# Kernel tuning notes

Measured on AMD Instinct MI355X. Metric: run time of the kernel, lower is better.

Reference implementation:

```python
import jax, jax.numpy as jnp
import numpy as np

N = 50000   # nodes
HID = 32    # hidden_channels
H = 8       # heads == num_edge_features (positional-arg aliasing in source)
E = 800000  # message-passing edges
L = 100000  # supervision (label) edges
NEG_SLOPE = 0.2


def gat_layer(x, src, dst, edge_attr, W, a_src, a_dst, We, a_e, b):
    # x: [N, Fin]; W: [Fin, H*C] -> out [N, H*C] (concat heads), PyG GATConv math
    C = W.shape[1] // H
    h = (x @ W).reshape(-1, H, C)                 # [N, H, C]
    al_src = (h * a_src).sum(-1)                  # [N, H]
    al_dst = (h * a_dst).sum(-1)                  # [N, H]
    he = (edge_attr @ We).reshape(-1, H, C)       # [E, H, C]
    al_e = (he * a_e).sum(-1)                     # [E, H]
    alpha = al_src[src] + al_dst[dst] + al_e      # [E, H]
    alpha = jax.nn.leaky_relu(alpha, NEG_SLOPE)
    # segment softmax over destination-node neighborhoods
    amax = jax.ops.segment_max(alpha, dst, num_segments=N)
    amax = jnp.where(jnp.isfinite(amax), amax, 0.0)
    ex = jnp.exp(alpha - amax[dst])
    denom = jax.ops.segment_sum(ex, dst, num_segments=N)
    w = ex / (denom[dst] + 1e-16)                 # [E, H]
    out = jax.ops.segment_sum(h[src] * w[:, :, None], dst, num_segments=N)
    return out.reshape(-1, H * C) + b             # [N, H*C]


def setup_inputs():
    key = jax.random.key(0)
    ks = jax.random.split(key, 24)
    s = 0.1
    d = {}
    d["node_ids"] = jax.random.randint(ks[0], (N,), 0, N)
    d["edge_index"] = jax.random.randint(ks[1], (2, E), 0, N)
    d["edge_label_index"] = jax.random.randint(ks[2], (2, L), 0, N)
    d["topic"] = jax.random.randint(ks[3], (1,), 0, 10)
    d["edge_attr"] = jax.random.normal(ks[4], (E, H))
    d["edge_label_attr"] = jax.random.normal(ks[5], (L, H))
    d["emb"] = jax.random.normal(ks[6], (N, HID)) * s
    d["W1"] = jax.random.normal(ks[7], (HID, H * HID)) * s
    d["a_src1"] = jax.random.normal(ks[8], (H, HID)) * s
    d["a_dst1"] = jax.random.normal(ks[9], (H, HID)) * s
    d["We1"] = jax.random.normal(ks[10], (H, H * HID)) * s
    d["a_e1"] = jax.random.normal(ks[11], (H, HID)) * s
    d["b1"] = jnp.zeros((H * HID,))
    d["lin1_W"] = jax.random.normal(ks[12], (H * HID, HID)) * s
    d["lin1_b"] = jnp.zeros((HID,))
    d["W2"] = jax.random.normal(ks[13], (HID, H * HID)) * s
    d["a_src2"] = jax.random.normal(ks[14], (H, HID)) * s
    d["a_dst2"] = jax.random.normal(ks[15], (H, HID)) * s
    d["We2"] = jax.random.normal(ks[16], (H, H * HID)) * s
    d["a_e2"] = jax.random.normal(ks[17], (H, HID)) * s
    d["b2"] = jnp.zeros((H * HID,))
    d["lin5_W"] = jax.random.normal(ks[18], (H * HID, H)) * s
    d["lin5_b"] = jnp.zeros((H,))
    d["clf_W"] = jax.random.normal(ks[19], (2 * H, H)) * s
    d["clf_b"] = jnp.zeros((H,))
    return d


def reference(node_ids, edge_index, edge_label_index, topic, edge_attr, edge_label_attr, emb, W1, a_src1, a_dst1, We1, a_e1, b1, lin1_W, lin1_b, W2, a_src2, a_dst2, We2, a_e2, b2, lin5_W, lin5_b, clf_W, clf_b):
    src, dst = edge_index[0], edge_index[1]
    x = emb[node_ids]                                                   # [N, HID]
    x = jax.nn.relu(gat_layer(x, src, dst, edge_attr, W1, a_src1, a_dst1, We1, a_e1, b1))
    x = x @ lin1_W + lin1_b                                             # dropout(p=0.1) is identity in eval
    x = jax.nn.relu(gat_layer(x, src, dst, edge_attr, W2, a_src2, a_dst2, We2, a_e2, b2))
    x = x @ lin5_W + lin5_b                                             # [N, H]
    fu = x[edge_label_index[0]]                                         # [L, H]
    fm = x[edge_label_index[1]]                                         # [L, H]
    fu = jnp.concatenate([fu, edge_label_attr], axis=-1) @ clf_W + clf_b
    return jax.nn.sigmoid((fu * fm).sum(-1))                            # [L]
```

## Files before the change

### kernel.cpp

```cpp
#include <hip/hip_runtime.h>
#include <hip/hip_bf16.h>

#define HC    256
#define FIN   32
#define NH    8
#define GROUP 8
#define CAPW  32

typedef __hip_bfloat16 bf16;

__device__ __forceinline__ float blo(unsigned int u) { return __uint_as_float(u << 16); }
__device__ __forceinline__ float bhi(unsigned int u) { return __uint_as_float(u & 0xffff0000u); }

__global__ void count_kernel(const int* __restrict__ dst, int* __restrict__ cnt, int E_) {
  int e = blockIdx.x * blockDim.x + threadIdx.x;
  if (e < E_) atomicAdd(&cnt[dst[e]], 1);
}

__global__ __launch_bounds__(256) void
scan_partial(const int* __restrict__ cnt, int* __restrict__ tmp,
             int* __restrict__ bsum, int N_) {
  __shared__ int part[256];
  int t = threadIdx.x, i = blockIdx.x * 256 + t;
  int v = (i < N_) ? cnt[i] : 0;
  part[t] = v;
  __syncthreads();
#pragma unroll
  for (int off = 1; off < 256; off <<= 1) {
    int u = (t >= off) ? part[t - off] : 0;
    __syncthreads();
    part[t] += u;
    __syncthreads();
  }
  if (i < N_) tmp[i] = part[t];
  if (t == 255) bsum[blockIdx.x] = part[255];
}

__global__ __launch_bounds__(1024) void
scan_bsum(int* __restrict__ bsum, int NB) {
  __shared__ int part[1024];
  int t = threadIdx.x;
  int v = (t < NB) ? bsum[t] : 0;
  part[t] = v;
  __syncthreads();
  for (int off = 1; off < 1024; off <<= 1) {
    int u = (t >= off) ? part[t - off] : 0;
    __syncthreads();
    part[t] += u;
    __syncthreads();
  }
  if (t < NB) bsum[t] = part[t] - v;
}

__global__ __launch_bounds__(256) void
scan_final(const int* __restrict__ cnt, const int* __restrict__ tmp,
           const int* __restrict__ bsum, int* __restrict__ rowptr,
           int* __restrict__ fill, int N_, int E_) {
  int t = threadIdx.x, i = blockIdx.x * 256 + t;
  if (i < N_) {
    int ex = bsum[blockIdx.x] + tmp[i] - cnt[i];
    rowptr[i] = ex;
    fill[i] = ex;
  }
  if (i == 0) rowptr[N_] = E_;
}

__global__ void scatter_kernel(const int* __restrict__ src, const int* __restrict__ dst,
                               int* __restrict__ fill, const float* __restrict__ edge_attr,
                               const float* __restrict__ M,
                               int* __restrict__ srcs, float* __restrict__ ale1,
                               float* __restrict__ ale2, int E_) {
  __shared__ float Msh[128];
  if (threadIdx.x < 128) Msh[threadIdx.x] = M[threadIdx.x];
  __syncthreads();
  int e = blockIdx.x * blockDim.x + threadIdx.x;
  if (e < E_) {
    int pos = atomicAdd(&fill[dst[e]], 1);
    srcs[pos] = src[e];
    const float4* ep = (const float4*)(edge_attr + (size_t)e * NH);
    float4 a0 = ep[0], a1 = ep[1];
    float ea[8] = {a0.x, a0.y, a0.z, a0.w, a1.x, a1.y, a1.z, a1.w};
    float o1[8], o2[8];
#pragma unroll
    for (int h = 0; h < 8; ++h) { o1[h] = 0.f; o2[h] = 0.f; }
#pragma unroll
    for (int k = 0; k < 8; ++k) {
      float x = ea[k];
#pragma unroll
      for (int h = 0; h < 8; ++h) {
        o1[h] = fmaf(x, Msh[k * 8 + h], o1[h]);
        o2[h] = fmaf(x, Msh[64 + k * 8 + h], o2[h]);
      }
    }
    float4* p1 = (float4*)(ale1 + (size_t)pos * NH);
    p1[0] = make_float4(o1[0], o1[1], o1[2], o1[3]);
    p1[1] = make_float4(o1[4], o1[5], o1[6], o1[7]);
    float4* p2 = (float4*)(ale2 + (size_t)pos * NH);
    p2[0] = make_float4(o2[0], o2[1], o2[2], o2[3]);
    p2[1] = make_float4(o2[4], o2[5], o2[6], o2[7]);
  }
}

__global__ void fold_kernel(const float* __restrict__ We1, const float* __restrict__ ae1,
                            const float* __restrict__ We2, const float* __restrict__ ae2,
                            const float* __restrict__ W1, const float* __restrict__ as1,
                            const float* __restrict__ ad1,
                            const float* __restrict__ W2, const float* __restrict__ as2,
                            const float* __restrict__ ad2,
                            float* __restrict__ M) {
  for (int idx = threadIdx.x; idx < 1152; idx += 256) {
    const float* A; const float* V; int i;
    if (idx < 64)       { i = idx;       A = We1; V = ae1; }
    else if (idx < 128) { i = idx - 64;  A = We2; V = ae2; }
    else if (idx < 384) { i = idx - 128; A = W1;  V = as1; }
    else if (idx < 640) { i = idx - 384; A = W1;  V = ad1; }
    else if (idx < 896) { i = idx - 640; A = W2;  V = as2; }
    else                { i = idx - 896; A = W2;  V = ad2; }
    int k = i >> 3, h = i & 7;
    float s = 0.f;
    for (int c = 0; c < FIN; ++c)
      s = fmaf(A[k * HC + h * FIN + c], V[h * FIN + c], s);
    M[idx] = s;
  }
}

__global__ __launch_bounds__(256) void
prep1_kernel(const float* __restrict__ emb, const int* __restrict__ node_ids,
             const float* __restrict__ P,
             bf16* __restrict__ xq, float* __restrict__ alsrc,
             float* __restrict__ aldst, int N_) {
  __shared__ float xs[8][33];
  int t = threadIdx.x, n0 = blockIdx.x * 8;
  int nl = t >> 5, c = t & 31;
  int n = n0 + nl;
  if (n < N_) {
    float v = emb[(size_t)node_ids[n] * FIN + c];
    xq[(size_t)n * FIN + c] = __float2bfloat16(v);
    xs[nl][c] = v;
  }
  __syncthreads();
  if (t < 64) {
    int nl2 = t >> 3, h = t & 7;
    int n2 = n0 + nl2;
    if (n2 < N_) {
      float sa = 0.f, sd = 0.f;
#pragma unroll
      for (int k = 0; k < FIN; ++k) {
        float x = xs[nl2][k];
        sa = fmaf(x, P[k * 8 + h], sa);
        sd = fmaf(x, P[256 + k * 8 + h], sd);
      }
      alsrc[(size_t)n2 * NH + h] = sa;
      aldst[(size_t)n2 * NH + h] = sd;
    }
  }
}

template <int K, int LOG2K, bool LOGITS>
__global__ __launch_bounds__(256, 8) void
agg_kernel(const int* __restrict__ rowptr, const int* __restrict__ srcs,
           const float* __restrict__ ale,
           const float* __restrict__ alsrc, const float* __restrict__ aldst,
           const bf16* __restrict__ xq,
           const float* __restrict__ W, const float* __restrict__ b,
           const float* __restrict__ Wlin, const float* __restrict__ blin,
           float* __restrict__ xoutf, bf16* __restrict__ xqn,
           const float* __restrict__ Pn,
           float* __restrict__ alsrcn, float* __restrict__ aldstn, int N_) {
  __shared__ __align__(16) char smem[17408];
  unsigned int* xsu = (unsigned int*)smem;
  float* wsf   = (float*)(smem + 8192);
  float* ald_s = (float*)(smem + 12288);
  float* zs   = (float*)smem;
  float* gs   = (float*)(smem + 8192);
  float* red  = (float*)smem;
  float* xrow = (float*)(smem + 16384);

  int t = threadIdx.x;
  int n0 = blockIdx.x * GROUP;
  int w = t >> 6, l = t & 63, h = l >> 3, q = l & 7;

  unsigned int* xw  = xsu + w * 512;
  float*        wsw = wsf + w * 256;

  int nA = n0 + w * 2;
  int e0  = rowptr[(nA     <= N_) ? nA     : N_];
  int e1  = rowptr[(nA + 1 <= N_) ? nA + 1 : N_];
  int e2g = rowptr[(nA + 2 <= N_) ? nA + 2 : N_];

  if (t < GROUP * NH) {
    int nn = n0 + (t >> 3);
    ald_s[t] = (nn < N_) ? aldst[(size_t)nn * NH + (t & 7)] : 0.f;
  }
  __syncthreads();

  float4 acc0 = make_float4(0.f, 0.f, 0.f, 0.f);
  float4 acc1 = make_float4(0.f, 0.f, 0.f, 0.f);
  float dn0 = 0.f, dn1 = 0.f;

  for (int cbeg = e0; cbeg < e2g; cbeg += CAPW) {
    int clen = e2g - cbeg; if (clen > CAPW) clen = CAPW;

    int ntask = clen * 8;
    for (int idx = l; idx < ntask; idx += 64) {
      int e = idx >> 3, c4 = idx & 7;
      int s = srcs[cbeg + e];
      uint2 v = *(const uint2*)(xq + (size_t)s * FIN + c4 * 4);
      *(uint2*)&xw[e * 16 + c4 * 2] = v;
    }
    {
      int e2 = l >> 1, half = l & 1;
      if (e2 < clen) {
        int j = cbeg + e2;
        int ii = (j >= e1) ? 1 : 0;
        int sn = srcs[j];
        float4 av  = *(const float4*)(ale + (size_t)j * NH + half * 4);
        float4 as4 = *(const float4*)(alsrc + (size_t)sn * NH + half * 4);
        float4 ad4 = *(const float4*)&ald_s[(w * 2 + ii) * 8 + half * 4];
        float o[4];
        float a0f = av.x + as4.x + ad4.x; a0f = (a0f >= 0.f) ? a0f : 0.2f * a0f;
        float a1f = av.y + as4.y + ad4.y; a1f = (a1f >= 0.f) ? a1f : 0.2f * a1f;
        float a2f = av.z + as4.z + ad4.z; a2f = (a2f >= 0.f) ? a2f : 0.2f * a2f;
        float a3f = av.w + as4.w + ad4.w; a3f = (a3f >= 0.f) ? a3f : 0.2f * a3f;
        o[0] = __expf(a0f); o[1] = __expf(a1f); o[2] = __expf(a2f); o[3] = __expf(a3f);
        *(float4*)&wsw[e2 * 8 + half * 4] = make_float4(o[0], o[1], o[2], o[3]);
      }
    }
    asm volatile("s_waitcnt lgkmcnt(0)" ::: "memory");

    int hA = e1 - cbeg; if (hA < 0) hA = 0; if (hA > clen) hA = clen;
#pragma unroll 4
    for (int le = 0; le < hA; ++le) {
      float wv = wsw[le * 8 + h];
      uint2 u = *(const uint2*)&xw[le * 16 + q * 2];
      acc0.x = fmaf(blo(u.x), wv, acc0.x);
      acc0.y = fmaf(bhi(u.x), wv, acc0.y);
      acc0.z = fmaf(blo(u.y), wv, acc0.z);
      acc0.w = fmaf(bhi(u.y), wv, acc0.w);
      dn0 += wv;
    }
#pragma unroll 4
    for (int le = hA; le < clen; ++le) {
      float wv = wsw[le * 8 + h];
      uint2 u = *(const uint2*)&xw[le * 16 + q * 2];
      acc1.x = fmaf(blo(u.x), wv, acc1.x);
      acc1.y = fmaf(bhi(u.x), wv, acc1.y);
      acc1.z = fmaf(blo(u.y), wv, acc1.z);
      acc1.w = fmaf(bhi(u.y), wv, acc1.w);
      dn1 += wv;
    }
    asm volatile("s_waitcnt lgkmcnt(0)" ::: "memory");
  }

  float rd0 = 1.0f / (dn0 + 1e-16f);
  float rd1 = 1.0f / (dn1 + 1e-16f);
  *(float4*)&zs[(w * 2 + 0) * 256 + l * 4] =
      make_float4(acc0.x * rd0, acc0.y * rd0, acc0.z * rd0, acc0.w * rd0);
  *(float4*)&zs[(w * 2 + 1) * 256 + l * 4] =
      make_float4(acc1.x * rd1, acc1.y * rd1, acc1.z * rd1, acc1.w * rd1);
  __syncthreads();

  int hE = t >> 5;
  float g[GROUP];
#pragma unroll
  for (int i = 0; i < GROUP; ++i) g[i] = b[t];
#pragma unroll
  for (int k4 = 0; k4 < 8; ++k4) {
    float za[GROUP][4];
#pragma unroll
    for (int i = 0; i < GROUP; ++i)
      *(float4*)za[i] = *(const float4*)&zs[i * 256 + hE * 32 + k4 * 4];
#pragma unroll
    for (int kk = 0; kk < 4; ++kk) {
      float wv = W[(k4 * 4 + kk) * HC + t];
#pragma unroll
      for (int i = 0; i < GROUP; ++i) g[i] = fmaf(za[i][kk], wv, g[i]);
    }
  }
  __syncthreads();
#pragma unroll
  for (int i = 0; i < GROUP; ++i) gs[i * 256 + t] = (g[i] > 0.f) ? g[i] : 0.f;
  __syncthreads();

  {
    int kk = t & (K - 1), r = t >> LOG2K;
    float part[GROUP];
#pragma unroll
    for (int i = 0; i < GROUP; ++i) part[i] = 0.f;
#pragma unroll
    for (int j4 = 0; j4 < K / 4; ++j4) {
      float ga[GROUP][4];
#pragma unroll
      for (int i = 0; i < GROUP; ++i)
        *(float4*)ga[i] = *(const float4*)&gs[i * 256 + r * K + j4 * 4];
#pragma unroll
      for (int jj = 0; jj < 4; ++jj) {
        float wl = Wlin[(r * K + j4 * 4 + jj) * K + kk];
#pragma unroll
        for (int i = 0; i < GROUP; ++i) part[i] = fmaf(ga[i][jj], wl, part[i]);
      }
    }
#pragma unroll
    for (int i = 0; i < GROUP; ++i) red[i * 256 + t] = part[i];
  }
  __syncthreads();

  if (LOGITS) {
    if (t < GROUP * 32) {
      int i = t >> 5, kk = t & 31;
      float s = blin[kk];
#pragma unroll
      for (int r2 = 0; r2 < HC / K; ++r2) s += red[i * 256 + r2 * K + kk];
      int nn = n0 + i;
      if (nn < N_) xqn[(size_t)nn * FIN + kk] = __float2bfloat16(s);
      xrow[t] = s;
    }
    __syncthreads();
    if (t < GROUP * NH) {
      int i = t >> 3, hh = t & 7;
      int nn = n0 + i;
      if (nn < N_) {
        float sa = 0.f, sd = 0.f;
#pragma unroll
        for (int k2 = 0; k2 < FIN; ++k2) {
          float x = xrow[i * 32 + k2];
          sa = fmaf(x, Pn[k2 * 8 + hh], sa);
          sd = fmaf(x, Pn[256 + k2 * 8 + hh], sd);
        }
        alsrcn[(size_t)nn * NH + hh] = sa;
        aldstn[(size_t)nn * NH + hh] = sd;
      }
    }
  } else {
    if (t < GROUP * K) {
      int i = t >> LOG2K, kk = t & (K - 1);
      float s = blin[kk];
#pragma unroll
      for (int r2 = 0; r2 < HC / K; ++r2) s += red[i * 256 + r2 * K + kk];
      int nn = n0 + i;
      if (nn < N_) xoutf[(size_t)nn * K + kk] = s;
    }
  }
}

__global__ void clf_kernel(const int* __restrict__ eli, const float* __restrict__ ela,
                           const float* __restrict__ x2, const float* __restrict__ clfW,
                           const float* __restrict__ clfb, float* __restrict__ out, int L_) {
  int i = blockIdx.x * blockDim.x + threadIdx.x;
  if (i >= L_) return;
  int u = eli[i], m = eli[L_ + i];
  const float4* xup = (const float4*)(x2 + (size_t)u * NH);
  const float4* xmp = (const float4*)(x2 + (size_t)m * NH);
  const float4* eap = (const float4*)(ela + (size_t)i * NH);
  float4 xu0 = xup[0], xu1 = xup[1];
  float4 xm0 = xmp[0], xm1 = xmp[1];
  float4 el0 = eap[0], el1 = eap[1];
  float xu[NH] = {xu0.x, xu0.y, xu0.z, xu0.w, xu1.x, xu1.y, xu1.z, xu1.w};
  float xm[NH] = {xm0.x, xm0.y, xm0.z, xm0.w, xm1.x, xm1.y, xm1.z, xm1.w};
  float el[NH] = {el0.x, el0.y, el0.z, el0.w, el1.x, el1.y, el1.z, el1.w};
  float fu[NH];
#pragma unroll
  for (int kk = 0; kk < NH; ++kk) fu[kk] = clfb[kk];
#pragma unroll
  for (int j = 0; j < NH; ++j) {
#pragma unroll
    for (int kk = 0; kk < NH; ++kk) fu[kk] = fmaf(xu[j], clfW[j * NH + kk], fu[kk]);
  }
#pragma unroll
  for (int j = 0; j < NH; ++j) {
#pragma unroll
    for (int kk = 0; kk < NH; ++kk) fu[kk] = fmaf(el[j], clfW[(NH + j) * NH + kk], fu[kk]);
  }
  float dot = 0.f;
#pragma unroll
  for (int kk = 0; kk < NH; ++kk) dot += fu[kk] * xm[kk];
  out[i] = 1.f / (1.f + expf(-dot));
}

extern "C" void kernel_launch(void* const* d_in, const int* in_sizes, int n_in,
                              void* d_out, int out_size, void* d_ws, size_t ws_size,
                              hipStream_t stream) {
  const int* node_ids   = (const int*)d_in[0];
  const int* edge_index = (const int*)d_in[1];
  const int* eli        = (const int*)d_in[2];
  const float* edge_attr = (const float*)d_in[4];
  const float* ela       = (const float*)d_in[5];
  const float* emb       = (const float*)d_in[6];
  const float* W1     = (const float*)d_in[7];
  const float* a_src1 = (const float*)d_in[8];
  const float* a_dst1 = (const float*)d_in[9];
  const float* We1    = (const float*)d_in[10];
  const float* a_e1   = (const float*)d_in[11];
  const float* b1     = (const float*)d_in[12];
  const float* lin1W  = (const float*)d_in[13];
  const float* lin1b  = (const float*)d_in[14];
  const float* W2     = (const float*)d_in[15];
  const float* a_src2 = (const float*)d_in[16];
  const float* a_dst2 = (const float*)d_in[17];
  const float* We2    = (const float*)d_in[18];
  const float* a_e2   = (const float*)d_in[19];
  const float* b2     = (const float*)d_in[20];
  const float* lin5W  = (const float*)d_in[21];
  const float* lin5b  = (const float*)d_in[22];
  const float* clfW   = (const float*)d_in[23];
  const float* clfb   = (const float*)d_in[24];

  const int N_ = in_sizes[0];
  const int E_ = in_sizes[1] / 2;
  const int L_ = in_sizes[2] / 2;
  const int* src  = edge_index;
  const int* dstp = edge_index + E_;

  char* p = (char*)d_ws;
  auto carve = [&](size_t bytes) -> char* {
    char* r = p;
    p += (bytes + 255) & ~(size_t)255;
    return r;
  };
  bf16*  xq1     = (bf16*)carve((size_t)N_ * FIN * 2);
  bf16*  xq2     = (bf16*)carve((size_t)N_ * FIN * 2);
  float* ale1_s  = (float*)carve((size_t)E_ * NH * 4);
  float* ale2_s  = (float*)carve((size_t)E_ * NH * 4);
  float* alsrc1  = (float*)carve((size_t)N_ * NH * 4);
  float* aldst1  = (float*)carve((size_t)N_ * NH * 4);
  float* alsrc2  = (float*)carve((size_t)N_ * NH * 4);
  float* aldst2  = (float*)carve((size_t)N_ * NH * 4);
  float* x2b     = (float*)carve((size_t)N_ * NH * 4);
  float* Mbuf    = (float*)carve(1152 * 4);
  int*   cnt     = (int*)carve((size_t)N_ * 4);
  int*   rowptr  = (int*)carve((size_t)(N_ + 1) * 4);
  int*   fill    = (int*)carve((size_t)N_ * 4);
  int*   stmp    = (int*)carve((size_t)N_ * 4);
  int*   bsum    = (int*)carve(1024 * 4);
  int*   srcs    = (int*)carve((size_t)E_ * 4);

  hipMemsetAsync(cnt, 0, (size_t)N_ * 4, stream);
  int eb = (E_ + 255) / 256;
  int nb = (N_ + 255) / 256;
  fold_kernel<<<1, 256, 0, stream>>>(We1, a_e1, We2, a_e2, W1, a_src1, a_dst1,
                                     W2, a_src2, a_dst2, Mbuf);
  count_kernel<<<eb, 256, 0, stream>>>(dstp, cnt, E_);
  scan_partial<<<nb, 256, 0, stream>>>(cnt, stmp, bsum, N_);
  scan_bsum<<<1, 1024, 0, stream>>>(bsum, nb);
  scan_final<<<nb, 256, 0, stream>>>(cnt, stmp, bsum, rowptr, fill, N_, E_);
  scatter_kernel<<<eb, 256, 0, stream>>>(src, dstp, fill, edge_attr, Mbuf,
                                         srcs, ale1_s, ale2_s, E_);
  prep1_kernel<<<(N_ + 7) / 8, 256, 0, stream>>>(emb, node_ids, Mbuf + 128,
                                                 xq1, alsrc1, aldst1, N_);

  int gb = (N_ + GROUP - 1) / GROUP;
  agg_kernel<32, 5, true><<<gb, 256, 0, stream>>>(
      rowptr, srcs, ale1_s, alsrc1, aldst1, xq1,
      W1, b1, lin1W, lin1b, nullptr, xq2, Mbuf + 640, alsrc2, aldst2, N_);

  agg_kernel<8, 3, false><<<gb, 256, 0, stream>>>(
      rowptr, srcs, ale2_s, alsrc2, aldst2, xq2,
      W2, b2, lin5W, lin5b, x2b, nullptr, nullptr, nullptr, nullptr, N_);

  clf_kernel<<<(L_ + 255) / 256, 256, 0, stream>>>(eli, ela, x2b, clfW, clfb,
                                                   (float*)d_out, L_);
}
```

Measured before the change: 365.5 us.

## Fuse preprocessing kernels, drop fill atomics, store edge logits as bf16

count_kernel now saves each edge's atomic slot order, so the scatter step can compute its CSR position as rowptr plus that order without a second atomic pass. The fold computation moves into the single-block bsum scan kernel, and the edge scatter and node prep are merged into one launch split by block index. Edge attention logits for both layers are packed as bf16 into one interleaved 32-byte record, halving that storage and its read traffic in the aggregation kernels. The trade-offs are an extra ord array write and read, and reduced precision on the edge logit term.

After: 330.2 us. -9.6%, faster.

```diff
diff --git a/kernel.cpp b/kernel.cpp
--- a/kernel.cpp
+++ b/kernel.cpp
@@ -11,10 +11,17 @@
 
 __device__ __forceinline__ float blo(unsigned int u) { return __uint_as_float(u << 16); }
 __device__ __forceinline__ float bhi(unsigned int u) { return __uint_as_float(u & 0xffff0000u); }
-
-__global__ void count_kernel(const int* __restrict__ dst, int* __restrict__ cnt, int E_) {
+__device__ __forceinline__ unsigned int pk2(float a, float b) {
+  bf16 ha = __float2bfloat16(a), hb = __float2bfloat16(b);
+  unsigned short ua, ub;
+  __builtin_memcpy(&ua, &ha, 2); __builtin_memcpy(&ub, &hb, 2);
+  return (unsigned int)ua | ((unsigned int)ub << 16);
+}
+
+__global__ void count_kernel(const int* __restrict__ dst, int* __restrict__ cnt,
+                             int* __restrict__ ord, int E_) {
   int e = blockIdx.x * blockDim.x + threadIdx.x;
-  if (e < E_) atomicAdd(&cnt[dst[e]], 1);
+  if (e < E_) ord[e] = atomicAdd(&cnt[dst[e]], 1);
 }
 
 __global__ __launch_bounds__(256) void
@@ -37,7 +44,14 @@
 }
 
 __global__ __launch_bounds__(1024) void
-scan_bsum(int* __restrict__ bsum, int NB) {
+scan_bsum_fold(int* __restrict__ bsum, int NB,
+               const float* __restrict__ We1, const float* __restrict__ ae1,
+               const float* __restrict__ We2, const float* __restrict__ ae2,
+               const float* __restrict__ W1, const float* __restrict__ as1,
+               const float* __restrict__ ad1,
+               const float* __restrict__ W2, const float* __restrict__ as2,
+               const float* __restrict__ ad2,
+               float* __restrict__ M) {
   __shared__ int part[1024];
   int t = threadIdx.x;
   int v = (t < NB) ? bsum[t] : 0;
@@ -50,65 +64,8 @@
     __syncthreads();
   }
   if (t < NB) bsum[t] = part[t] - v;
-}
-
-__global__ __launch_bounds__(256) void
-scan_final(const int* __restrict__ cnt, const int* __restrict__ tmp,
-           const int* __restrict__ bsum, int* __restrict__ rowptr,
-           int* __restrict__ fill, int N_, int E_) {
-  int t = threadIdx.x, i = blockIdx.x * 256 + t;
-  if (i < N_) {
-    int ex = bsum[blockIdx.x] + tmp[i] - cnt[i];
-    rowptr[i] = ex;
-    fill[i] = ex;
-  }
-  if (i == 0) rowptr[N_] = E_;
-}
-
-__global__ void scatter_kernel(const int* __restrict__ src, const int* __restrict__ dst,
-                               int* __restrict__ fill, const float* __restrict__ edge_attr,
-                               const float* __restrict__ M,
-                               int* __restrict__ srcs, float* __restrict__ ale1,
-                               float* __restrict__ ale2, int E_) {
-  __shared__ float Msh[128];
-  if (threadIdx.x < 128) Msh[threadIdx.x] = M[threadIdx.x];
-  __syncthreads();
-  int e = blockIdx.x * blockDim.x + threadIdx.x;
-  if (e < E_) {
-    int pos = atomicAdd(&fill[dst[e]], 1);
-    srcs[pos] = src[e];
-    const float4* ep = (const float4*)(edge_attr + (size_t)e * NH);
-    float4 a0 = ep[0], a1 = ep[1];
-    float ea[8] = {a0.x, a0.y, a0.z, a0.w, a1.x, a1.y, a1.z, a1.w};
-    float o1[8], o2[8];
-#pragma unroll
-    for (int h = 0; h < 8; ++h) { o1[h] = 0.f; o2[h] = 0.f; }
-#pragma unroll
-    for (int k = 0; k < 8; ++k) {
-      float x = ea[k];
-#pragma unroll
-      for (int h = 0; h < 8; ++h) {
-        o1[h] = fmaf(x, Msh[k * 8 + h], o1[h]);
-        o2[h] = fmaf(x, Msh[64 + k * 8 + h], o2[h]);
-      }
-    }
-    float4* p1 = (float4*)(ale1 + (size_t)pos * NH);
-    p1[0] = make_float4(o1[0], o1[1], o1[2], o1[3]);
-    p1[1] = make_float4(o1[4], o1[5], o1[6], o1[7]);
-    float4* p2 = (float4*)(ale2 + (size_t)pos * NH);
-    p2[0] = make_float4(o2[0], o2[1], o2[2], o2[3]);
-    p2[1] = make_float4(o2[4], o2[5], o2[6], o2[7]);
-  }
-}
-
-__global__ void fold_kernel(const float* __restrict__ We1, const float* __restrict__ ae1,
-                            const float* __restrict__ We2, const float* __restrict__ ae2,
-                            const float* __restrict__ W1, const float* __restrict__ as1,
-                            const float* __restrict__ ad1,
-                            const float* __restrict__ W2, const float* __restrict__ as2,
-                            const float* __restrict__ ad2,
-                            float* __restrict__ M) {
-  for (int idx = threadIdx.x; idx < 1152; idx += 256) {
+
+  for (int idx = t; idx < 1152; idx += 1024) {
     const float* A; const float* V; int i;
     if (idx < 64)       { i = idx;       A = We1; V = ae1; }
     else if (idx < 128) { i = idx - 64;  A = We2; V = ae2; }
@@ -125,33 +82,80 @@
 }
 
 __global__ __launch_bounds__(256) void
-prep1_kernel(const float* __restrict__ emb, const int* __restrict__ node_ids,
-             const float* __restrict__ P,
-             bf16* __restrict__ xq, float* __restrict__ alsrc,
-             float* __restrict__ aldst, int N_) {
+scan_final(const int* __restrict__ cnt, const int* __restrict__ tmp,
+           const int* __restrict__ bsum, int* __restrict__ rowptr,
+           int N_, int E_) {
+  int t = threadIdx.x, i = blockIdx.x * 256 + t;
+  if (i < N_) rowptr[i] = bsum[blockIdx.x] + tmp[i] - cnt[i];
+  if (i == 0) rowptr[N_] = E_;
+}
+
+__global__ __launch_bounds__(256) void
+scatter_prep_kernel(const int* __restrict__ src, const int* __restrict__ dst,
+                    const int* __restrict__ rowptr, const int* __restrict__ ord,
+                    const float* __restrict__ edge_attr, const float* __restrict__ M,
+                    int* __restrict__ srcs, unsigned int* __restrict__ alepk,
+                    const float* __restrict__ emb, const int* __restrict__ node_ids,
+                    bf16* __restrict__ xq, float* __restrict__ alsrc,
+                    float* __restrict__ aldst,
+                    int E_, int N_, int eb) {
+  __shared__ float Msh[128];
   __shared__ float xs[8][33];
-  int t = threadIdx.x, n0 = blockIdx.x * 8;
-  int nl = t >> 5, c = t & 31;
-  int n = n0 + nl;
-  if (n < N_) {
-    float v = emb[(size_t)node_ids[n] * FIN + c];
-    xq[(size_t)n * FIN + c] = __float2bfloat16(v);
-    xs[nl][c] = v;
-  }
-  __syncthreads();
-  if (t < 64) {
-    int nl2 = t >> 3, h = t & 7;
-    int n2 = n0 + nl2;
-    if (n2 < N_) {
-      float sa = 0.f, sd = 0.f;
-#pragma unroll
-      for (int k = 0; k < FIN; ++k) {
-        float x = xs[nl2][k];
-        sa = fmaf(x, P[k * 8 + h], sa);
-        sd = fmaf(x, P[256 + k * 8 + h], sd);
+  int t = threadIdx.x;
+  if (blockIdx.x < eb) {
+    if (t < 128) Msh[t] = M[t];
+    __syncthreads();
+    int e = blockIdx.x * 256 + t;
+    if (e < E_) {
+      int pos = rowptr[dst[e]] + ord[e];
+      srcs[pos] = src[e];
+      const float4* ep = (const float4*)(edge_attr + (size_t)e * NH);
+      float4 a0 = ep[0], a1 = ep[1];
+      float ea[8] = {a0.x, a0.y, a0.z, a0.w, a1.x, a1.y, a1.z, a1.w};
+      float o1[8], o2[8];
+#pragma unroll
+      for (int h = 0; h < 8; ++h) { o1[h] = 0.f; o2[h] = 0.f; }
+#pragma unroll
+      for (int k = 0; k < 8; ++k) {
+        float x = ea[k];
+#pragma unroll
+        for (int h = 0; h < 8; ++h) {
+          o1[h] = fmaf(x, Msh[k * 8 + h], o1[h]);
+          o2[h] = fmaf(x, Msh[64 + k * 8 + h], o2[h]);
+        }
       }
-      alsrc[(size_t)n2 * NH + h] = sa;
-      aldst[(size_t)n2 * NH + h] = sd;
+      uint4 r0 = make_uint4(pk2(o1[0], o1[1]), pk2(o1[2], o1[3]),
+                            pk2(o1[4], o1[5]), pk2(o1[6], o1[7]));
+      uint4 r1 = make_uint4(pk2(o2[0], o2[1]), pk2(o2[2], o2[3]),
+                            pk2(o2[4], o2[5]), pk2(o2[6], o2[7]));
+      uint4* op = (uint4*)(alepk + (size_t)pos * 8);
+      op[0] = r0; op[1] = r1;
+    }
+  } else {
+    const float* P = M + 128;
+    int n0 = (blockIdx.x - eb) * 8;
+    int nl = t >> 5, c = t & 31;
+    int n = n0 + nl;
+    if (n < N_) {
+      float v = emb[(size_t)node_ids[n] * FIN + c];
+      xq[(size_t)n * FIN + c] = __float2bfloat16(v);
+      xs[nl][c] = v;
+    }
+    __syncthreads();
+    if (t < 64) {
+      int nl2 = t >> 3, h = t & 7;
+      int n2 = n0 + nl2;
+      if (n2 < N_) {
+        float sa = 0.f, sd = 0.f;
+#pragma unroll
+        for (int k = 0; k < FIN; ++k) {
+          float x = xs[nl2][k];
+          sa = fmaf(x, P[k * 8 + h], sa);
+          sd = fmaf(x, P[256 + k * 8 + h], sd);
+        }
+        alsrc[(size_t)n2 * NH + h] = sa;
+        aldst[(size_t)n2 * NH + h] = sd;
+      }
     }
   }
 }
@@ -159,7 +163,7 @@
 template <int K, int LOG2K, bool LOGITS>
 __global__ __launch_bounds__(256, 8) void
 agg_kernel(const int* __restrict__ rowptr, const int* __restrict__ srcs,
-           const float* __restrict__ ale,
+           const bf16* __restrict__ ale,
            const float* __restrict__ alsrc, const float* __restrict__ aldst,
            const bf16* __restrict__ xq,
            const float* __restrict__ W, const float* __restrict__ b,
@@ -214,16 +218,15 @@
         int j = cbeg + e2;
         int ii = (j >= e1) ? 1 : 0;
         int sn = srcs[j];
-        float4 av  = *(const float4*)(ale + (size_t)j * NH + half * 4);
+        uint2 ue  = *(const uint2*)(ale + (size_t)j * 16 + half * 4);
         float4 as4 = *(const float4*)(alsrc + (size_t)sn * NH + half * 4);
         float4 ad4 = *(const float4*)&ald_s[(w * 2 + ii) * 8 + half * 4];
-        float o[4];
-        float a0f = av.x + as4.x + ad4.x; a0f = (a0f >= 0.f) ? a0f : 0.2f * a0f;
-        float a1f = av.y + as4.y + ad4.y; a1f = (a1f >= 0.f) ? a1f : 0.2f * a1f;
-        float a2f = av.z + as4.z + ad4.z; a2f = (a2f >= 0.f) ? a2f : 0.2f * a2f;
-        float a3f = av.w + as4.w + ad4.w; a3f = (a3f >= 0.f) ? a3f : 0.2f * a3f;
-        o[0] = __expf(a0f); o[1] = __expf(a1f); o[2] = __expf(a2f); o[3] = __expf(a3f);
-        *(float4*)&wsw[e2 * 8 + half * 4] = make_float4(o[0], o[1], o[2], o[3]);
+        float a0f = blo(ue.x) + as4.x + ad4.x; a0f = (a0f >= 0.f) ? a0f : 0.2f * a0f;
+        float a1f = bhi(ue.x) + as4.y + ad4.y; a1f = (a1f >= 0.f) ? a1f : 0.2f * a1f;
+        float a2f = blo(ue.y) + as4.z + ad4.z; a2f = (a2f >= 0.f) ? a2f : 0.2f * a2f;
+        float a3f = bhi(ue.y) + as4.w + ad4.w; a3f = (a3f >= 0.f) ? a3f : 0.2f * a3f;
+        *(float4*)&wsw[e2 * 8 + half * 4] =
+            make_float4(__expf(a0f), __expf(a1f), __expf(a2f), __expf(a3f));
       }
     }
     asm volatile("s_waitcnt lgkmcnt(0)" ::: "memory");
@@ -419,8 +422,7 @@
   };
   bf16*  xq1     = (bf16*)carve((size_t)N_ * FIN * 2);
   bf16*  xq2     = (bf16*)carve((size_t)N_ * FIN * 2);
-  float* ale1_s  = (float*)carve((size_t)E_ * NH * 4);
-  float* ale2_s  = (float*)carve((size_t)E_ * NH * 4);
+  unsigned int* alepk = (unsigned int*)carve((size_t)E_ * 32);
   float* alsrc1  = (float*)carve((size_t)N_ * NH * 4);
   float* aldst1  = (float*)carve((size_t)N_ * NH * 4);
   float* alsrc2  = (float*)carve((size_t)N_ * NH * 4);
@@ -429,32 +431,32 @@
   float* Mbuf    = (float*)carve(1152 * 4);
   int*   cnt     = (int*)carve((size_t)N_ * 4);
   int*   rowptr  = (int*)carve((size_t)(N_ + 1) * 4);
-  int*   fill    = (int*)carve((size_t)N_ * 4);
   int*   stmp    = (int*)carve((size_t)N_ * 4);
   int*   bsum    = (int*)carve(1024 * 4);
   int*   srcs    = (int*)carve((size_t)E_ * 4);
+  int*   ordb    = (int*)carve((size_t)E_ * 4);
 
   hipMemsetAsync(cnt, 0, (size_t)N_ * 4, stream);
   int eb = (E_ + 255) / 256;
   int nb = (N_ + 255) / 256;
-  fold_kernel<<<1, 256, 0, stream>>>(We1, a_e1, We2, a_e2, W1, a_src1, a_dst1,
-                                     W2, a_src2, a_dst2, Mbuf);
-  count_kernel<<<eb, 256, 0, stream>>>(dstp, cnt, E_);
+  int pb = (N_ + 7) / 8;
+  count_kernel<<<eb, 256, 0, stream>>>(dstp, cnt, ordb, E_);
   scan_partial<<<nb, 256, 0, stream>>>(cnt, stmp, bsum, N_);
-  scan_bsum<<<1, 1024, 0, stream>>>(bsum, nb);
-  scan_final<<<nb, 256, 0, stream>>>(cnt, stmp, bsum, rowptr, fill, N_, E_);
-  scatter_kernel<<<eb, 256, 0, stream>>>(src, dstp, fill, edge_attr, Mbuf,
-                                         srcs, ale1_s, ale2_s, E_);
-  prep1_kernel<<<(N_ + 7) / 8, 256, 0, stream>>>(emb, node_ids, Mbuf + 128,
-                                                 xq1, alsrc1, aldst1, N_);
+  scan_bsum_fold<<<1, 1024, 0, stream>>>(bsum, nb, We1, a_e1, We2, a_e2,
+                                         W1, a_src1, a_dst1, W2, a_src2, a_dst2,
+                                         Mbuf);
+  scan_final<<<nb, 256, 0, stream>>>(cnt, stmp, bsum, rowptr, N_, E_);
+  scatter_prep_kernel<<<eb + pb, 256, 0, stream>>>(
+      src, dstp, rowptr, ordb, edge_attr, Mbuf, srcs, alepk,
+      emb, node_ids, xq1, alsrc1, aldst1, E_, N_, eb);
 
   int gb = (N_ + GROUP - 1) / GROUP;
   agg_kernel<32, 5, true><<<gb, 256, 0, stream>>>(
-      rowptr, srcs, ale1_s, alsrc1, aldst1, xq1,
+      rowptr, srcs, (const bf16*)alepk, alsrc1, aldst1, xq1,
       W1, b1, lin1W, lin1b, nullptr, xq2, Mbuf + 640, alsrc2, aldst2, N_);
 
   agg_kernel<8, 3, false><<<gb, 256, 0, stream>>>(
-      rowptr, srcs, ale2_s, alsrc2, aldst2, xq2,
+      rowptr, srcs, ((const bf16*)alepk) + 8, alsrc2, aldst2, xq2,
       W2, b2, lin5W, lin5b, x2b, nullptr, nullptr, nullptr, nullptr, N_);
 
   clf_kernel<<<(L_ + 255) / 256, 256, 0, stream>>>(eli, ela, x2b, clfW, clfb,
```
